# Kernel optimization log

Hardware: AMD Instinct MI355X
Metric: run time of the kernel (lower is better)

The kernel has to match this reference:

```python
import jax, jax.numpy as jnp
import numpy as np

B = 64        # graphs per batch
N0 = 131072   # total nodes (2048 per graph)
E = 1048576   # total edges (within-graph)
H = 128       # hidden_size
C = 7         # class_num (input feature dim)
EPS = 1e-5


def setup_inputs() -> dict:
    key = jax.random.key(0)
    ks = jax.random.split(key, 16)
    n0 = N0 // B
    x = jax.random.normal(ks[0], (N0, C), dtype=jnp.float32)
    # within-graph random edges: edge e belongs to graph e // (E//B)
    g = jnp.repeat(jnp.arange(B, dtype=jnp.int32), E // B)
    row = jax.random.randint(ks[1], (E,), 0, n0, dtype=jnp.int32) + g * n0
    col = jax.random.randint(ks[2], (E,), 0, n0, dtype=jnp.int32) + g * n0
    edge_index = jnp.stack([row, col], axis=0)
    batch = jnp.repeat(jnp.arange(B, dtype=jnp.int32), n0)
    s = 0.05
    params = dict(
        Wc1=jax.random.normal(ks[3], (C, H), jnp.float32) * s,     # conv1 weight
        Wc=jax.random.normal(ks[4], (3, H, H), jnp.float32) * s,   # conv2-4 weights
        bc=jax.random.normal(ks[5], (4, H), jnp.float32) * s,      # conv biases
        Wf=jax.random.normal(ks[6], (4, H, H), jnp.float32) * s,   # fc weights
        bf=jax.random.normal(ks[7], (4, H), jnp.float32) * s,      # fc biases
        bn_g=jnp.ones((4, H), jnp.float32),                        # BN gamma
        bn_b=jnp.zeros((4, H), jnp.float32),                       # BN beta
        Ws1=jax.random.normal(ks[8], (4, H, 1), jnp.float32) * s,  # SAG GraphConv root weight
        Ws2=jax.random.normal(ks[9], (4, H, 1), jnp.float32) * s,  # SAG GraphConv neighbor weight
        bs=jax.random.normal(ks[10], (4, 1), jnp.float32) * s,     # SAG GraphConv bias
    )
    return dict(x=x, edge_index=edge_index, batch=batch, **params)


def _gcn_conv(x, W, b, row, col, m, N):
    # PyG GCNConv with self loops: out_i = sum_{j->i} h_j / sqrt(d_i d_j) + h_i / d_i + b
    h = x @ W
    deg = jax.ops.segment_sum(m, col, num_segments=N) + 1.0  # +1 for self loop
    dis = jax.lax.rsqrt(deg)
    norm = dis[row] * dis[col] * m  # masked-out edges contribute 0
    agg = jax.ops.segment_sum(h[row] * norm[:, None], col, num_segments=N)
    return agg + h * (dis * dis)[:, None] + b


def _sag_score(x, W1, W2, b, row, col, m, N):
    # GraphConv(H, 1, aggr='add'): score_i = W1^T x_i + W2^T sum_{j->i} x_j + b
    nbr = jax.ops.segment_sum(x[row] * m[:, None], col, num_segments=N)
    return (x @ W1 + nbr @ W2 + b).reshape(-1)


def _bn(x, g, b):
    mu = jnp.mean(x, axis=0)
    var = jnp.mean((x - mu) ** 2, axis=0)  # biased, matches torch BN training
    return (x - mu) * jax.lax.rsqrt(var + EPS) * g + b


def reference(x, edge_index, batch, Wc1, Wc, bc, Wf, bf, bn_g, bn_b, Ws1, Ws2, bs):
    row, col = edge_index[0], edge_index[1]
    m = jnp.ones(row.shape, x.dtype)  # edge validity mask (static-size edge list)
    n = x.shape[0] // B               # nodes per graph (equal-size graphs)
    for i in range(4):
        N = B * n
        W = Wc1 if i == 0 else Wc[i - 1]
        h = _gcn_conv(x, W, bc[i], row, col, m, N)
        h = jax.nn.relu(h @ Wf[i] + bf[i])
        h = _bn(h, bn_g[i], bn_b[i])
        # SAGPooling(ratio=0.5): per-graph top-k by GraphConv score, x *= tanh(score)
        score = _sag_score(h, Ws1[i], Ws2[i], bs[i], row, col, m, N)
        k = n // 2
        _, idx = jax.lax.top_k(score.reshape(B, n), k)  # [B, k] per-graph indices
        perm = (idx + jnp.arange(B, dtype=idx.dtype)[:, None] * n).reshape(-1)
        x = h[perm] * jnp.tanh(score[perm])[:, None]
        # re-index edges; mask edges touching removed nodes
        inv = jnp.full((N,), -1, dtype=row.dtype).at[perm].set(
            jnp.arange(B * k, dtype=row.dtype))
        nr, nc = inv[row], inv[col]
        valid = (nr >= 0) & (nc >= 0)
        m = m * valid.astype(m.dtype)
        row = jnp.where(valid, nr, 0)
        col = jnp.where(valid, nc, 0)
        n = k
    # global_mean_pool over block-structured batch -> [B, H]
    return x.reshape(B, n, -1).mean(axis=1)
```

## Files before the change

### kernel.cpp

```cpp
#include <hip/hip_runtime.h>
#include <cstdint>

#define HB 128
#define NB 64
#define NE 1048576
#define SLAB 16384
#define XP 132

typedef float v2f __attribute__((ext_vector_type(2)));

__global__ __launch_bounds__(256) void init_edges_k(const int* __restrict__ ei,
    int* __restrict__ row, int* __restrict__ col, int* __restrict__ gcnt0, int E) {
  int e = blockIdx.x * blockDim.x + threadIdx.x;
  if (e < E) { row[e] = ei[e]; col[e] = ei[E + e]; }
  if (blockIdx.x == 0 && threadIdx.x < NB) gcnt0[threadIdx.x] = SLAB;
}

__global__ __launch_bounds__(256) void conv_fc0_k(const float* __restrict__ aggx,
    const float* __restrict__ Wc1, const float* __restrict__ bc0,
    const float* __restrict__ Wf, const float* __restrict__ bf0,
    float* __restrict__ out, int N, float* __restrict__ stat) {
  __shared__ float lt[64][128];
  __shared__ float laggx[64][8];
  __shared__ float lwc1[7 * 128];
  float2 (*red)[128] = (float2(*)[128])lt;
  int tid = threadIdx.x;
  int tx = tid & 31, ty = tid >> 5;
  long rowbase = (long)blockIdx.x * 64;
  for (int i = tid; i < 7 * 32; i += 256)
    ((float4*)lwc1)[i] = ((const float4*)Wc1)[i];
  if (tid < 128) {
    int lr = tid >> 1, lq = (tid & 1) * 4;
    *(float4*)&laggx[lr][lq] = *(const float4*)(aggx + (rowbase + lr) * 8 + lq);
  }
  __syncthreads();
  float4 tacc[8];
  float4 bcv = ((const float4*)bc0)[tx];
  #pragma unroll
  for (int r = 0; r < 8; ++r) tacc[r] = bcv;
  #pragma unroll
  for (int k = 0; k < 7; ++k) {
    float4 wv = ((float4*)lwc1)[k * 32 + tx];
    #pragma unroll
    for (int r = 0; r < 8; ++r) {
      float xv = laggx[ty + 8 * r][k];
      tacc[r].x += xv * wv.x; tacc[r].y += xv * wv.y;
      tacc[r].z += xv * wv.z; tacc[r].w += xv * wv.w;
    }
  }
  #pragma unroll
  for (int r = 0; r < 8; ++r)
    *(float4*)&lt[ty + 8 * r][4 * tx] = tacc[r];
  __syncthreads();
  v2f acc2[16];
  #pragma unroll
  for (int r = 0; r < 16; ++r) acc2[r] = (v2f){0.f, 0.f};
  for (int kc = 0; kc < 16; ++kc) {
    float4 wreg[8];
    #pragma unroll
    for (int k = 0; k < 8; ++k)
      wreg[k] = *(const float4*)(Wf + (size_t)(kc * 8 + k) * HB + 4 * tx);
    #pragma unroll
    for (int kk = 0; kk < 8; kk += 4) {
      float4 xreg[8];
      #pragma unroll
      for (int r = 0; r < 8; ++r)
        xreg[r] = *(const float4*)&lt[ty + 8 * r][kc * 8 + kk];
      #pragma unroll
      for (int k2 = 0; k2 < 4; ++k2) {
        float4 wv = wreg[kk + k2];
        v2f wlo = {wv.x, wv.y}, whi = {wv.z, wv.w};
        #pragma unroll
        for (int r = 0; r < 8; ++r) {
          float xv = ((const float*)&xreg[r])[k2];
          v2f xvv = {xv, xv};
          acc2[2 * r]     += xvv * wlo;
          acc2[2 * r + 1] += xvv * whi;
        }
      }
    }
  }
  float4 bv = ((const float4*)bf0)[tx];
  float4 psum = make_float4(0.f, 0.f, 0.f, 0.f);
  float4 psq  = make_float4(0.f, 0.f, 0.f, 0.f);
  __syncthreads();
  #pragma unroll
  for (int r = 0; r < 8; ++r) {
    float4 v;
    v.x = fmaxf(acc2[2 * r].x + bv.x, 0.f);
    v.y = fmaxf(acc2[2 * r].y + bv.y, 0.f);
    v.z = fmaxf(acc2[2 * r + 1].x + bv.z, 0.f);
    v.w = fmaxf(acc2[2 * r + 1].y + bv.w, 0.f);
    psum.x += v.x; psum.y += v.y; psum.z += v.z; psum.w += v.w;
    psq.x += v.x * v.x; psq.y += v.y * v.y;
    psq.z += v.z * v.z; psq.w += v.w * v.w;
    *(float4*)(out + (size_t)(rowbase + ty + 8 * r) * HB + 4 * tx) = v;
  }
  red[ty][4 * tx + 0] = make_float2(psum.x, psq.x);
  red[ty][4 * tx + 1] = make_float2(psum.y, psq.y);
  red[ty][4 * tx + 2] = make_float2(psum.z, psq.z);
  red[ty][4 * tx + 3] = make_float2(psum.w, psq.w);
  __syncthreads();
  if (tid < 128) {
    float s = 0.f, q = 0.f;
    #pragma unroll
    for (int t = 0; t < 8; ++t) { s += red[t][tid].x; q += red[t][tid].y; }
    float* st = stat + ((blockIdx.x & 7) << 8);
    atomicAdd(&st[tid], s);
    atomicAdd(&st[128 + tid], q);
  }
}

__global__ __launch_bounds__(256) void conv_fc_k(const float* __restrict__ Ap,
    const float* __restrict__ bnsc, const int* __restrict__ sel,
    const float* __restrict__ scale, const int* __restrict__ srow,
    const float* __restrict__ snorm, const int* __restrict__ off,
    const int* __restrict__ offe, const float* __restrict__ dis,
    const float* __restrict__ Wc, const float* __restrict__ bc0,
    const float* __restrict__ Wf, const float* __restrict__ bf0,
    float* __restrict__ out, int N, float* __restrict__ stat) {
  __shared__ float buf[64][XP];
  float2 (*red)[128] = (float2(*)[128])buf;
  int tid = threadIdx.x;
  int tx = tid & 31, ty = tid >> 5;
  long cpx = gridDim.x >> 3;
  long bb = ((long)blockIdx.x & 7) * cpx + ((long)blockIdx.x >> 3);
  long rowbase = bb * 64;
  {
    int r = tid >> 2;
    int chq = (tid & 3) * 32;
    int node = rowbase + r;
    float4 av[8], bv8[8];
    #pragma unroll
    for (int q = 0; q < 8; ++q) {
      av[q]  = *(const float4*)(bnsc + chq + 4 * q);
      bv8[q] = *(const float4*)(bnsc + 128 + chq + 4 * q);
    }
    int e0 = off[node], e1 = offe[node];
    float dv = dis[node];
    float4 acc[8];
    {
      float sc = scale[node] * dv * dv;
      const float* xr = Ap + (size_t)sel[node] * HB + chq;
      #pragma unroll
      for (int q = 0; q < 8; ++q) {
        float4 v = *(const float4*)(xr + 4 * q);
        acc[q].x = (v.x * av[q].x + bv8[q].x) * sc;
        acc[q].y = (v.y * av[q].y + bv8[q].y) * sc;
        acc[q].z = (v.z * av[q].z + bv8[q].z) * sc;
        acc[q].w = (v.w * av[q].w + bv8[q].w) * sc;
      }
    }
    for (int j = e0; j < e1; ++j) {
      int srcn = srow[j];
      float sc = snorm[j] * scale[srcn];
      const float* xr = Ap + (size_t)sel[srcn] * HB + chq;
      #pragma unroll
      for (int q = 0; q < 8; ++q) {
        float4 v = *(const float4*)(xr + 4 * q);
        acc[q].x += (v.x * av[q].x + bv8[q].x) * sc;
        acc[q].y += (v.y * av[q].y + bv8[q].y) * sc;
        acc[q].z += (v.z * av[q].z + bv8[q].z) * sc;
        acc[q].w += (v.w * av[q].w + bv8[q].w) * sc;
      }
    }
    #pragma unroll
    for (int q = 0; q < 8; ++q) *(float4*)&buf[r][chq + 4 * q] = acc[q];
  }
  __syncthreads();
  {
    float4 bcv = ((const float4*)bc0)[tx];
    v2f acc2[16];
    #pragma unroll
    for (int r = 0; r < 8; ++r) {
      acc2[2 * r]     = (v2f){bcv.x, bcv.y};
      acc2[2 * r + 1] = (v2f){bcv.z, bcv.w};
    }
    for (int kc = 0; kc < 16; ++kc) {
      float4 wreg[8];
      #pragma unroll
      for (int k = 0; k < 8; ++k)
        wreg[k] = *(const float4*)(Wc + (size_t)(kc * 8 + k) * HB + 4 * tx);
      #pragma unroll
      for (int kk = 0; kk < 8; kk += 4) {
        float4 xreg[8];
        #pragma unroll
        for (int r = 0; r < 8; ++r)
          xreg[r] = *(const float4*)&buf[ty + 8 * r][kc * 8 + kk];
        #pragma unroll
        for (int k2 = 0; k2 < 4; ++k2) {
          float4 wv = wreg[kk + k2];
          v2f wlo = {wv.x, wv.y}, whi = {wv.z, wv.w};
          #pragma unroll
          for (int r = 0; r < 8; ++r) {
            float xv = ((const float*)&xreg[r])[k2];
            v2f xvv = {xv, xv};
            acc2[2 * r]     += xvv * wlo;
            acc2[2 * r + 1] += xvv * whi;
          }
        }
      }
    }
    __syncthreads();
    #pragma unroll
    for (int r = 0; r < 8; ++r) {
      float4 v;
      v.x = acc2[2 * r].x;     v.y = acc2[2 * r].y;
      v.z = acc2[2 * r + 1].x; v.w = acc2[2 * r + 1].y;
      *(float4*)&buf[ty + 8 * r][4 * tx] = v;
    }
  }
  __syncthreads();
  v2f acc2[16];
  #pragma unroll
  for (int r = 0; r < 16; ++r) acc2[r] = (v2f){0.f, 0.f};
  for (int kc = 0; kc < 16; ++kc) {
    float4 wreg[8];
    #pragma unroll
    for (int k = 0; k < 8; ++k)
      wreg[k] = *(const float4*)(Wf + (size_t)(kc * 8 + k) * HB + 4 * tx);
    #pragma unroll
    for (int kk = 0; kk < 8; kk += 4) {
      float4 xreg[8];
      #pragma unroll
      for (int r = 0; r < 8; ++r)
        xreg[r] = *(const float4*)&buf[ty + 8 * r][kc * 8 + kk];
      #pragma unroll
      for (int k2 = 0; k2 < 4; ++k2) {
        float4 wv = wreg[kk + k2];
        v2f wlo = {wv.x, wv.y}, whi = {wv.z, wv.w};
        #pragma unroll
        for (int r = 0; r < 8; ++r) {
          float xv = ((const float*)&xreg[r])[k2];
          v2f xvv = {xv, xv};
          acc2[2 * r]     += xvv * wlo;
          acc2[2 * r + 1] += xvv * whi;
        }
      }
    }
  }
  float4 bv = ((const float4*)bf0)[tx];
  float4 psum = make_float4(0.f, 0.f, 0.f, 0.f);
  float4 psq  = make_float4(0.f, 0.f, 0.f, 0.f);
  __syncthreads();
  #pragma unroll
  for (int r = 0; r < 8; ++r) {
    float4 v;
    v.x = fmaxf(acc2[2 * r].x + bv.x, 0.f);
    v.y = fmaxf(acc2[2 * r].y + bv.y, 0.f);
    v.z = fmaxf(acc2[2 * r + 1].x + bv.z, 0.f);
    v.w = fmaxf(acc2[2 * r + 1].y + bv.w, 0.f);
    psum.x += v.x; psum.y += v.y; psum.z += v.z; psum.w += v.w;
    psq.x += v.x * v.x; psq.y += v.y * v.y;
    psq.z += v.z * v.z; psq.w += v.w * v.w;
    *(float4*)(out + (size_t)(rowbase + ty + 8 * r) * HB + 4 * tx) = v;
  }
  red[ty][4 * tx + 0] = make_float2(psum.x, psq.x);
  red[ty][4 * tx + 1] = make_float2(psum.y, psq.y);
  red[ty][4 * tx + 2] = make_float2(psum.z, psq.z);
  red[ty][4 * tx + 3] = make_float2(psum.w, psq.w);
  __syncthreads();
  if (tid < 128) {
    float s = 0.f, q = 0.f;
    #pragma unroll
    for (int t = 0; t < 8; ++t) { s += red[t][tid].x; q += red[t][tid].y; }
    float* st = stat + (((int)blockIdx.x & 7) << 8);
    atomicAdd(&st[tid], s);
    atomicAdd(&st[128 + tid], q);
  }
}

__global__ __launch_bounds__(1024) void csr_build_k(const int* __restrict__ row,
    const int* __restrict__ col, const int* __restrict__ gcnt,
    float* __restrict__ dis, int* __restrict__ off, int* __restrict__ offe,
    int* __restrict__ srow, float* __restrict__ snorm, int n) {
  extern __shared__ int lds[];
  int* ldeg = lds;
  int* lsa  = lds + n;
  int* lsb  = lds + 2 * n;
  float* ldis = (float*)(lds + 3 * n);
  int g = blockIdx.x, tid = threadIdx.x;
  int e0 = g * SLAB, e1 = e0 + gcnt[g];
  int base = g * n;
  for (int i = tid; i < n; i += 1024) ldeg[i] = 0;
  __syncthreads();
  for (int e = e0 + tid; e < e1; e += 1024) atomicAdd(&ldeg[col[e] - base], 1);
  __syncthreads();
  for (int i = tid; i < n; i += 1024) {
    int d = ldeg[i];
    ldis[i] = rsqrtf((float)d + 1.f);
    lsa[i] = d;
  }
  __syncthreads();
  int* src = lsa; int* dst = lsb;
  for (int o = 1; o < n; o <<= 1) {
    for (int i = tid; i < n; i += 1024) dst[i] = src[i] + ((i >= o) ? src[i - o] : 0);
    __syncthreads();
    int* t = src; src = dst; dst = t;
  }
  for (int i = tid; i < n; i += 1024) {
    int d = ldeg[i];
    int ex = src[i] - d;
    off[base + i]  = e0 + ex;
    offe[base + i] = e0 + ex + d;
    ldeg[i] = ex;
    dis[base + i] = ldis[i];
  }
  __syncthreads();
  for (int e = e0 + tid; e < e1; e += 1024) {
    int r = row[e], c = col[e];
    int lc = c - base;
    int p = e0 + atomicAdd(&ldeg[lc], 1);
    srow[p] = r;
    snorm[p] = ldis[r - base] * ldis[lc];
  }
}

__global__ __launch_bounds__(256) void agg7_k(const float* __restrict__ x,
    const int* __restrict__ srow, const float* __restrict__ snorm,
    const int* __restrict__ off, const int* __restrict__ offe,
    const float* __restrict__ dis, float* __restrict__ aggx, int N) {
  int cpx = gridDim.x >> 3;
  int b = blockIdx.x;
  int bid = (b & 7) * cpx + (b >> 3);
  int gid = bid * 256 + threadIdx.x;
  int node = gid >> 3, c = gid & 7;
  if (node >= N) return;
  float acc = 0.f;
  if (c < 7) {
    int s = off[node], e = offe[node];
    for (int j = s; j < e; ++j) acc += x[(size_t)srow[j] * 7 + c] * snorm[j];
    float d = dis[node];
    acc += x[(size_t)node * 7 + c] * d * d;
  }
  aggx[(size_t)node * 8 + c] = acc;
}

__global__ __launch_bounds__(128) void bnfin_k(const float* __restrict__ stat8,
    const float* __restrict__ g, const float* __restrict__ b,
    float* __restrict__ sc, int N) {
  int c = threadIdx.x;
  if (c < 128) {
    float s = 0.f, q = 0.f;
    #pragma unroll
    for (int sh = 0; sh < 8; ++sh) {
      s += stat8[sh * 256 + c];
      q += stat8[sh * 256 + 128 + c];
    }
    float mu = s / N;
    float var = q / N - mu * mu;
    float a = g[c] * rsqrtf(var + 1e-5f);
    sc[c] = a;
    sc[128 + c] = b[c] - mu * a;
  }
}

__global__ __launch_bounds__(256) void score_prep_k(const float* __restrict__ h,
    const float* __restrict__ sc, const float* __restrict__ w1,
    const float* __restrict__ w2, float* __restrict__ selfs,
    float* __restrict__ t2, int N) {
  int gid = blockIdx.x * blockDim.x + threadIdx.x;
  int node = gid >> 6;
  if (node >= N) return;
  int lane = gid & 63, c = lane * 2;
  float2 v = *(const float2*)(h + (size_t)node * HB + c);
  v.x = v.x * sc[c] + sc[128 + c];
  v.y = v.y * sc[c + 1] + sc[128 + c + 1];
  float s1 = v.x * w1[c] + v.y * w1[c + 1];
  float s2 = v.x * w2[c] + v.y * w2[c + 1];
  #pragma unroll
  for (int off = 32; off > 0; off >>= 1) {
    s1 += __shfl_xor(s1, off);
    s2 += __shfl_xor(s2, off);
  }
  if (lane == 0) { selfs[node] = s1; t2[node] = s2; }
}

__global__ __launch_bounds__(256) void score_k(const float* __restrict__ selfs,
    const float* __restrict__ t2, const int* __restrict__ srow,
    const int* __restrict__ off, const int* __restrict__ offe,
    const float* __restrict__ bs, float* __restrict__ score, int N) {
  int i = blockIdx.x * blockDim.x + threadIdx.x;
  if (i >= N) return;
  float s = selfs[i] + bs[0];
  int e0 = off[i], e1 = offe[i];
  for (int j = e0; j < e1; ++j) s += t2[srow[j]];
  score[i] = s;
}

__global__ __launch_bounds__(256) void rank_topk_k(const float* __restrict__ score,
    int* __restrict__ inv, int* __restrict__ sel, float* __restrict__ scale,
    int n, int k, int bpg) {
  extern __shared__ float ls[];
  int g = blockIdx.x / bpg, sub = blockIdx.x % bpg;
  int tid = threadIdx.x;
  const float* sg = score + (size_t)g * n;
  for (int i = tid; i < n; i += 256) ls[i] = sg[i];
  __syncthreads();
  int i0 = sub * 256 + tid;
  float s0 = ls[i0];
  int r0 = 0;
  for (int jb = 0; jb < n; jb += 4) {
    float4 v = *(const float4*)(ls + jb);
    r0 += (v.x > s0) || (v.x == s0 && (jb + 0) < i0);
    r0 += (v.y > s0) || (v.y == s0 && (jb + 1) < i0);
    r0 += (v.z > s0) || (v.z == s0 && (jb + 2) < i0);
    r0 += (v.w > s0) || (v.w == s0 && (jb + 3) < i0);
  }
  if (r0 < k) {
    inv[(size_t)g * n + i0] = g * k + r0;
    sel[(size_t)g * k + r0] = g * n + i0;
    scale[(size_t)g * k + r0] = tanhf(s0);
  } else inv[(size_t)g * n + i0] = -1;
}

__global__ __launch_bounds__(256) void gather_x_k(const float* __restrict__ h,
    const float* __restrict__ bnsc, const int* __restrict__ sel,
    const float* __restrict__ scale, float* __restrict__ xout, int M) {
  int gid = blockIdx.x * blockDim.x + threadIdx.x;
  int r = gid >> 5;
  if (r >= M) return;
  int ch = (gid & 31) * 4;
  int old = sel[r];
  float sc = scale[r];
  float4 v = *(const float4*)(h + (size_t)old * HB + ch);
  float4 a = *(const float4*)(bnsc + ch);
  float4 b = *(const float4*)(bnsc + 128 + ch);
  v.x = (v.x * a.x + b.x) * sc; v.y = (v.y * a.y + b.y) * sc;
  v.z = (v.z * a.z + b.z) * sc; v.w = (v.w * a.w + b.w) * sc;
  *(float4*)(xout + (size_t)r * HB + ch) = v;
}

__global__ __launch_bounds__(256) void cmp_k(const int* __restrict__ row,
    const int* __restrict__ col, const int* __restrict__ inv,
    const int* __restrict__ gcntCur, int* __restrict__ nrow,
    int* __restrict__ ncol, int* __restrict__ gcntNxt) {
  int g = blockIdx.x >> 6;
  int eloc = ((blockIdx.x & 63) << 8) + threadIdx.x;
  int cnt = gcntCur[g];
  if (((blockIdx.x & 63) << 8) >= cnt) return;
  long e = (long)g * SLAB + eloc;
  bool valid = false; int nr = 0, nc = 0;
  if (eloc < cnt) {
    nr = inv[row[e]]; nc = inv[col[e]];
    valid = (nr >= 0) && (nc >= 0);
  }
  unsigned long long mask = __ballot(valid);
  int lane = threadIdx.x & 63, wid = threadIdx.x >> 6;
  __shared__ int ws[4];
  __shared__ int base;
  if (lane == 0) ws[wid] = __popcll(mask);
  __syncthreads();
  if (threadIdx.x == 0) {
    int a = ws[0], b = ws[1], c2 = ws[2], d = ws[3];
    int tot = a + b + c2 + d;
    base = tot ? atomicAdd(&gcntNxt[g], tot) : 0;
    ws[0] = 0; ws[1] = a; ws[2] = a + b; ws[3] = a + b + c2;
  }
  __syncthreads();
  if (valid) {
    unsigned long long lt = ((unsigned long long)1 << lane) - 1;
    long o = (long)g * SLAB + base + ws[wid] + (int)__popcll(mask & lt);
    nrow[o] = nr;
    ncol[o] = nc;
  }
}

__global__ __launch_bounds__(128) void pool_k(const float* __restrict__ x,
    float* __restrict__ out, int n) {
  int g = blockIdx.x, c = threadIdx.x;
  float s = 0.f;
  for (int r = 0; r < n; ++r) s += x[((size_t)g * n + r) * HB + c];
  out[g * HB + c] = s / n;
}

extern "C" void kernel_launch(void* const* d_in, const int* in_sizes, int n_in,
                              void* d_out, int out_size, void* d_ws, size_t ws_size,
                              hipStream_t stream) {
  const float* x_in = (const float*)d_in[0];
  const int*   ei   = (const int*)d_in[1];
  const float* Wc1  = (const float*)d_in[3];
  const float* Wc   = (const float*)d_in[4];
  const float* bc   = (const float*)d_in[5];
  const float* Wf   = (const float*)d_in[6];
  const float* bf   = (const float*)d_in[7];
  const float* bng  = (const float*)d_in[8];
  const float* bnb  = (const float*)d_in[9];
  const float* Ws1  = (const float*)d_in[10];
  const float* Ws2  = (const float*)d_in[11];
  const float* bs   = (const float*)d_in[12];

  const int N0 = 131072, E = NE;
  char* p = (char*)d_ws;
  auto alloc = [&](size_t bytes) -> char* {
    char* r = p; p += (bytes + 255) & ~(size_t)255; return r;
  };
  float* A    = (float*)alloc((size_t)N0 * HB * 4);
  float* Bb   = (float*)alloc((size_t)N0 * HB * 4);
  float* Cc   = (float*)alloc((size_t)(N0 / 2) * HB * 4);
  float* aggx = (float*)alloc((size_t)N0 * 8 * 4);
  int*   rowA = (int*)alloc((size_t)E * 4);
  int*   colA = (int*)alloc((size_t)E * 4);
  int*   rowB = (int*)alloc((size_t)E * 4);
  int*   colB = (int*)alloc((size_t)E * 4);
  float* dis  = (float*)alloc((size_t)N0 * 4);
  float* selfs= (float*)alloc((size_t)N0 * 4);
  float* t2v  = (float*)alloc((size_t)N0 * 4);
  float* score= (float*)alloc((size_t)N0 * 4);
  int*   inv  = (int*)alloc((size_t)N0 * 4);
  int*   off  = (int*)alloc((size_t)N0 * 4);
  int*   offe = (int*)alloc((size_t)N0 * 4);
  int*   sel  = (int*)alloc((size_t)(N0 / 2) * 4);
  float* scale= (float*)alloc((size_t)(N0 / 2) * 4);
  int*   gcntL= (int*)alloc(4 * NB * 4);
  float* stat8= (float*)alloc(4 * 8 * 256 * 4);
  float* bnsc = (float*)alloc(256 * 4);

  hipMemsetAsync(stat8, 0, 4 * 8 * 256 * 4, stream);
  hipMemsetAsync(gcntL, 0, 4 * NB * 4, stream);

  init_edges_k<<<E / 256, 256, 0, stream>>>(ei, rowA, colA, gcntL, E);

  int* rowCur = rowA; int* colCur = colA;
  int* rowNxt = rowB; int* colNxt = colB;

  int n = 2048;
  for (int i = 0; i < 4; ++i) {
    int N = NB * n, khalf = n >> 1;
    float* statL = stat8 + (size_t)i * 8 * 256;
    const float* Xin  = (i == 2) ? Bb : A;
    float*       Xout = (i == 0 || i == 2) ? A : Bb;
    int*   srow  = rowNxt;
    float* snorm = (float*)colNxt;
    csr_build_k<<<NB, 1024, (size_t)16 * n, stream>>>(
        rowCur, colCur, gcntL + i * NB, dis, off, offe, srow, snorm, n);
    if (i == 0) {
      agg7_k<<<N / 32, 256, 0, stream>>>(x_in, srow, snorm, off, offe, dis, aggx, N);
      conv_fc0_k<<<N / 64, 256, 0, stream>>>(aggx, Wc1, bc, Wf, bf, Xout, N, statL);
    } else {
      conv_fc_k<<<N / 64, 256, 0, stream>>>(
          Xin, bnsc, sel, scale, srow, snorm, off, offe, dis,
          Wc + (size_t)(i - 1) * HB * HB, bc + (size_t)i * HB,
          Wf + (size_t)i * HB * HB, bf + (size_t)i * HB, Xout, N, statL);
    }
    bnfin_k<<<1, 128, 0, stream>>>(statL, bng + (size_t)i * HB, bnb + (size_t)i * HB, bnsc, N);
    score_prep_k<<<N / 4, 256, 0, stream>>>(
        Xout, bnsc, Ws1 + (size_t)i * HB, Ws2 + (size_t)i * HB, selfs, t2v, N);
    score_k<<<(N + 255) / 256, 256, 0, stream>>>(
        selfs, t2v, srow, off, offe, bs + i, score, N);
    int bpg = n / 256;
    rank_topk_k<<<NB * bpg, 256, (size_t)n * 4, stream>>>(
        score, inv, sel, scale, n, khalf, bpg);
    if (i < 3) {
      cmp_k<<<NB * 64, 256, 0, stream>>>(rowCur, colCur, inv, gcntL + i * NB,
                                         rowNxt, colNxt, gcntL + (i + 1) * NB);
      int* t;
      t = rowCur; rowCur = rowNxt; rowNxt = t;
      t = colCur; colCur = colNxt; colNxt = t;
    } else {
      gather_x_k<<<(NB * khalf) / 8, 256, 0, stream>>>(
          Xout, bnsc, sel, scale, Cc, NB * khalf);
    }
    n = khalf;
  }
  pool_k<<<NB, 128, 0, stream>>>(Cc, (float*)d_out, n);
}
```

Baseline: 582.4 us.

## Hoist BN affine out of edge gather and precompute source indices in CSR

Uses linearity to apply the batch-norm scale/shift once after aggregation, tracking the sum of edge weights instead of applying the affine per edge. The CSR build now writes the resolved source row (sel[r]) and a weight premultiplied by the pooling scale, so the conv gather loop drops two dependent indirect loads per edge. This adds an extra edge-sized index array and more gathers in the CSR build kernel.

```diff
diff --git a/kernel.cpp b/kernel.cpp
--- a/kernel.cpp
+++ b/kernel.cpp
@@ -113,8 +113,8 @@
 
 __global__ __launch_bounds__(256) void conv_fc_k(const float* __restrict__ Ap,
     const float* __restrict__ bnsc, const int* __restrict__ sel,
-    const float* __restrict__ scale, const int* __restrict__ srow,
-    const float* __restrict__ snorm, const int* __restrict__ off,
+    const float* __restrict__ scale, const int* __restrict__ srowA,
+    const float* __restrict__ snorm2, const int* __restrict__ off,
     const int* __restrict__ offe, const float* __restrict__ dis,
     const float* __restrict__ Wc, const float* __restrict__ bc0,
     const float* __restrict__ Wf, const float* __restrict__ bf0,
@@ -130,42 +130,43 @@
     int r = tid >> 2;
     int chq = (tid & 3) * 32;
     int node = rowbase + r;
-    float4 av[8], bv8[8];
-    #pragma unroll
-    for (int q = 0; q < 8; ++q) {
-      av[q]  = *(const float4*)(bnsc + chq + 4 * q);
-      bv8[q] = *(const float4*)(bnsc + 128 + chq + 4 * q);
-    }
     int e0 = off[node], e1 = offe[node];
     float dv = dis[node];
     float4 acc[8];
+    float ssum;
     {
       float sc = scale[node] * dv * dv;
+      ssum = sc;
       const float* xr = Ap + (size_t)sel[node] * HB + chq;
       #pragma unroll
       for (int q = 0; q < 8; ++q) {
         float4 v = *(const float4*)(xr + 4 * q);
-        acc[q].x = (v.x * av[q].x + bv8[q].x) * sc;
-        acc[q].y = (v.y * av[q].y + bv8[q].y) * sc;
-        acc[q].z = (v.z * av[q].z + bv8[q].z) * sc;
-        acc[q].w = (v.w * av[q].w + bv8[q].w) * sc;
+        acc[q].x = v.x * sc; acc[q].y = v.y * sc;
+        acc[q].z = v.z * sc; acc[q].w = v.w * sc;
       }
     }
     for (int j = e0; j < e1; ++j) {
-      int srcn = srow[j];
-      float sc = snorm[j] * scale[srcn];
-      const float* xr = Ap + (size_t)sel[srcn] * HB + chq;
+      float sc = snorm2[j];
+      const float* xr = Ap + (size_t)srowA[j] * HB + chq;
+      ssum += sc;
       #pragma unroll
       for (int q = 0; q < 8; ++q) {
         float4 v = *(const float4*)(xr + 4 * q);
-        acc[q].x += (v.x * av[q].x + bv8[q].x) * sc;
-        acc[q].y += (v.y * av[q].y + bv8[q].y) * sc;
-        acc[q].z += (v.z * av[q].z + bv8[q].z) * sc;
-        acc[q].w += (v.w * av[q].w + bv8[q].w) * sc;
+        acc[q].x += v.x * sc; acc[q].y += v.y * sc;
+        acc[q].z += v.z * sc; acc[q].w += v.w * sc;
       }
     }
     #pragma unroll
-    for (int q = 0; q < 8; ++q) *(float4*)&buf[r][chq + 4 * q] = acc[q];
+    for (int q = 0; q < 8; ++q) {
+      float4 a  = *(const float4*)(bnsc + chq + 4 * q);
+      float4 b8 = *(const float4*)(bnsc + 128 + chq + 4 * q);
+      float4 o;
+      o.x = a.x * acc[q].x + b8.x * ssum;
+      o.y = a.y * acc[q].y + b8.y * ssum;
+      o.z = a.z * acc[q].z + b8.z * ssum;
+      o.w = a.w * acc[q].w + b8.w * ssum;
+      *(float4*)&buf[r][chq + 4 * q] = o;
+    }
   }
   __syncthreads();
   {
@@ -272,8 +273,10 @@
 
 __global__ __launch_bounds__(1024) void csr_build_k(const int* __restrict__ row,
     const int* __restrict__ col, const int* __restrict__ gcnt,
+    const int* __restrict__ sel, const float* __restrict__ scale,
     float* __restrict__ dis, int* __restrict__ off, int* __restrict__ offe,
-    int* __restrict__ srow, float* __restrict__ snorm, int n) {
+    int* __restrict__ srow, int* __restrict__ srowA,
+    float* __restrict__ snorm, int n) {
   extern __shared__ int lds[];
   int* ldeg = lds;
   int* lsa  = lds + n;
@@ -312,7 +315,9 @@
     int lc = c - base;
     int p = e0 + atomicAdd(&ldeg[lc], 1);
     srow[p] = r;
-    snorm[p] = ldis[r - base] * ldis[lc];
+    float nm = ldis[r - base] * ldis[lc];
+    if (sel) { srowA[p] = sel[r]; snorm[p] = nm * scale[r]; }
+    else     { srowA[p] = r;      snorm[p] = nm; }
   }
 }
 
@@ -503,6 +508,7 @@
   int*   colA = (int*)alloc((size_t)E * 4);
   int*   rowB = (int*)alloc((size_t)E * 4);
   int*   colB = (int*)alloc((size_t)E * 4);
+  int*   srowA= (int*)alloc((size_t)E * 4);
   float* dis  = (float*)alloc((size_t)N0 * 4);
   float* selfs= (float*)alloc((size_t)N0 * 4);
   float* t2v  = (float*)alloc((size_t)N0 * 4);
@@ -533,13 +539,14 @@
     int*   srow  = rowNxt;
     float* snorm = (float*)colNxt;
     csr_build_k<<<NB, 1024, (size_t)16 * n, stream>>>(
-        rowCur, colCur, gcntL + i * NB, dis, off, offe, srow, snorm, n);
+        rowCur, colCur, gcntL + i * NB, (i == 0) ? nullptr : sel,
+        (i == 0) ? nullptr : scale, dis, off, offe, srow, srowA, snorm, n);
     if (i == 0) {
       agg7_k<<<N / 32, 256, 0, stream>>>(x_in, srow, snorm, off, offe, dis, aggx, N);
       conv_fc0_k<<<N / 64, 256, 0, stream>>>(aggx, Wc1, bc, Wf, bf, Xout, N, statL);
     } else {
       conv_fc_k<<<N / 64, 256, 0, stream>>>(
-          Xin, bnsc, sel, scale, srow, snorm, off, offe, dis,
+          Xin, bnsc, sel, scale, srowA, snorm, off, offe, dis,
           Wc + (size_t)(i - 1) * HB * HB, bc + (size_t)i * HB,
           Wf + (size_t)i * HB * HB, bf + (size_t)i * HB, Xout, N, statL);
     }
```

Measured after the change: 601.6 us. +3.3%, slower.
